# Performance work log

Hardware: AMD Instinct MI355X
Metric: run time of the kernel (lower is better)

Reference implementation:

```python
import jax, jax.numpy as jnp
import numpy as np

EPS = 1e-5

def conv2d(x, w, stride, pad):
    return jax.lax.conv_general_dilated(
        x, w, window_strides=(stride, stride),
        padding=[(pad, pad), (pad, pad)],
        dimension_numbers=('NCHW', 'OIHW', 'NCHW'))

def batchnorm(x, gamma, beta, mean, var):
    # inference-mode BN over channel dim of NCHW
    inv = jax.lax.rsqrt(var + EPS)
    return (x - mean[None, :, None, None]) * (inv * gamma)[None, :, None, None] + beta[None, :, None, None]

def rational(x, num, den):
    # Rational activation, version A, degrees (5,4):
    #   P(x) = num0 + num1*x + ... + num5*x^5  (Horner)
    #   Q(x) = 1 + sum_{j=1..4} |den_{j-1}| * |x|^j
    p = num[5]
    for i in range(4, -1, -1):
        p = p * x + num[i]
    xa = jnp.abs(x)
    q = jnp.ones_like(x)
    pw = xa
    for j in range(4):
        q = q + jnp.abs(den[j]) * pw
        pw = pw * xa
    return p / q

def multi_variant_rationals(out, num_r, den_r, num_g, den_g, num_b, den_b):
    # channels 0::3 -> r, 1::3 -> g, 2::3 -> b, then re-interleave
    B, C, H, W = out.shape
    o = out.reshape(B, C // 3, 3, H, W)  # channel c = 3*j + k
    r = rational(o[:, :, 0], num_r, den_r)
    g = rational(o[:, :, 1], num_g, den_g)
    b = rational(o[:, :, 2], num_b, den_b)
    return jnp.stack([r, g, b], axis=2).reshape(B, C, H, W)

def setup_inputs() -> dict:
    key = jax.random.key(0)
    ks = jax.random.split(key, 12)
    B, Cin, Cout, H, W = 64, 96, 192, 56, 56
    inp = {
        'x': jax.random.normal(ks[0], (B, Cin, H, W), jnp.float32),
        'w1': jax.random.normal(ks[1], (Cout, Cin, 3, 3), jnp.float32) * 0.05,
        'gamma1': jnp.ones((Cout,), jnp.float32),
        'beta1': jnp.zeros((Cout,), jnp.float32),
        'mean1': jnp.zeros((Cout,), jnp.float32),
        'var1': jnp.ones((Cout,), jnp.float32),
        'num_r': jax.random.normal(ks[2], (6,), jnp.float32) * 0.3,
        'den_r': jax.random.normal(ks[3], (4,), jnp.float32) * 0.3,
        'num_g': jax.random.normal(ks[4], (6,), jnp.float32) * 0.3,
        'den_g': jax.random.normal(ks[5], (4,), jnp.float32) * 0.3,
        'num_b': jax.random.normal(ks[6], (6,), jnp.float32) * 0.3,
        'den_b': jax.random.normal(ks[7], (4,), jnp.float32) * 0.3,
        'w2': jax.random.normal(ks[8], (Cout, Cout, 3, 3), jnp.float32) * 0.05,
        'gamma2': jnp.ones((Cout,), jnp.float32),
        'beta2': jnp.zeros((Cout,), jnp.float32),
        'mean2': jnp.zeros((Cout,), jnp.float32),
        'var2': jnp.ones((Cout,), jnp.float32),
        'ws': jax.random.normal(ks[9], (Cout, Cin, 1, 1), jnp.float32) * 0.05,
        'gammas': jnp.ones((Cout,), jnp.float32),
        'betas': jnp.zeros((Cout,), jnp.float32),
        'means': jnp.zeros((Cout,), jnp.float32),
        'vars_': jnp.ones((Cout,), jnp.float32),
    }
    return inp

def reference(x, w1, gamma1, beta1, mean1, var1,
              num_r, den_r, num_g, den_g, num_b, den_b,
              w2, gamma2, beta2, mean2, var2,
              ws, gammas, betas, means, vars_):
    STRIDE = 2
    out = batchnorm(conv2d(x, w1, STRIDE, 1), gamma1, beta1, mean1, var1)
    out = multi_variant_rationals(out, num_r, den_r, num_g, den_g, num_b, den_b)
    out = batchnorm(conv2d(out, w2, 1, 1), gamma2, beta2, mean2, var2)
    shortcut = batchnorm(conv2d(x, ws, STRIDE, 0), gammas, betas, means, vars_)
    out = out + shortcut
    out = multi_variant_rationals(out, num_r, den_r, num_g, den_g, num_b, den_b)
    return out
```

## Files before the change

kernel.cpp:

```cpp
#include <hip/hip_runtime.h>

#define EPSBN  1e-5f
#define NBLK_A 392
#define NBLK_B 392

#define W1B_OFF 0u
#define W2B_OFF 331776u
#define WSB_OFF 995328u
#define CS_OFF  1044480u
#define XT_OFF  1048320u
#define ACT_OFF 39583488u

typedef __attribute__((ext_vector_type(8))) short bf16x8;
typedef __attribute__((ext_vector_type(4))) short bf16x4;
typedef __attribute__((ext_vector_type(4))) float f32x4;

#define WAITV(N) asm volatile("s_waitcnt vmcnt(" #N ")" ::: "memory")

__device__ __forceinline__ short f2bf(float f) {
    unsigned u = __float_as_uint(f);
    u += 0x7fffu + ((u >> 16) & 1u);
    return (short)(u >> 16);
}

__device__ __forceinline__ void gload16(const short* g, short* l) {
    __builtin_amdgcn_global_load_lds(
        (const __attribute__((address_space(1))) void*)g,
        (__attribute__((address_space(3))) void*)l, 16, 0, 0);
}

__device__ __forceinline__ float rational_eval(float v, const float* nm, const float* dn) {
    float p = nm[5];
    p = p * v + nm[4];
    p = p * v + nm[3];
    p = p * v + nm[2];
    p = p * v + nm[1];
    p = p * v + nm[0];
    float xa = fabsf(v);
    float q = 1.0f;
    float pw = xa;
    q += dn[0] * pw; pw *= xa;
    q += dn[1] * pw; pw *= xa;
    q += dn[2] * pw; pw *= xa;
    q += dn[3] * pw;
    float inv = __builtin_amdgcn_rcpf(q);
    inv = inv * (2.0f - q * inv);
    return p * inv;
}

__device__ __forceinline__ void sel_coeffs(int v, const float cnm[3][6], const float cdn[3][4],
                                           float nm[6], float dn[4]) {
#pragma unroll
    for (int i = 0; i < 6; i++) nm[i] = (v == 0) ? cnm[0][i] : ((v == 1) ? cnm[1][i] : cnm[2][i]);
#pragma unroll
    for (int i = 0; i < 4; i++) dn[i] = (v == 0) ? cdn[0][i] : ((v == 1) ? cdn[1][i] : cdn[2][i]);
}

extern "C" __global__ __launch_bounds__(256)
void prep_all_kernel(
    const float* __restrict__ x,
    const float* __restrict__ w1, const float* __restrict__ w2, const float* __restrict__ wsc,
    const float* g1, const float* b1, const float* m1, const float* v1,
    const float* g2, const float* b2, const float* m2, const float* v2,
    const float* gs, const float* bs, const float* ms, const float* vs,
    short* __restrict__ w1t, short* __restrict__ w2t, short* __restrict__ wst,
    float* __restrict__ cs, short* __restrict__ act, short* __restrict__ xt)
{
    __shared__ float t[96 * 57];
    int blk = blockIdx.x;
    if (blk < 1296) {
        int i = blk * 256 + threadIdx.x;
        int u = i / 12288; int L = i - u * 12288;
        int row = L >> 6; int s = (L >> 3) & 7; int j = L & 7;
        int k = u * 64 + ((s ^ (row & 7)) << 3) + j;
        int kpos = k / 192; int ci = k - kpos * 192;
        float a = g2[row] * rsqrtf(v2[row] + EPSBN);
        w2t[i] = f2bf(w2[(row * 192 + ci) * 9 + kpos] * a);
    } else if (blk < 1944) {
        int i = (blk - 1296) * 256 + threadIdx.x;
        int u = i / 6144; int L = i - u * 6144;
        int row = L >> 5; int s = (L >> 3) & 3; int j = L & 7;
        int k = u * 32 + ((s ^ ((row >> 1) & 3)) << 3) + j;
        int kpos = k / 96; int ci = k - kpos * 96;
        float a = g1[row] * rsqrtf(v1[row] + EPSBN);
        w1t[i] = f2bf(w1[(row * 96 + ci) * 9 + kpos] * a);
    } else if (blk < 2040) {
        int i = (blk - 1944) * 256 + threadIdx.x;
        int u = i / 12288; int L = i - u * 12288;
        int row = L >> 6; int s = (L >> 3) & 7; int j = L & 7;
        int k = u * 64 + ((s ^ (row & 7)) << 3) + j;
        float a = gs[row] * rsqrtf(vs[row] + EPSBN);
        wst[i] = (k < 96) ? f2bf(wsc[row * 96 + k] * a) : (short)0;
    } else if (blk < 3432) {
        int i = (blk - 2040) * 256 + threadIdx.x;
        int c4 = i % 48;
        int tt = i / 48;
        int rp = tt % 116;
        int n = tt / 116;
        int h, w;
        if (rp < 30)      { h = 0;  w = rp; }
        else if (rp < 60) { h = 29; w = rp - 30; }
        else { int k = rp - 60; h = (k >> 1) + 1; w = (k & 1) ? 29 : 0; }
        *(bf16x4*)&act[((n * 30 + h) * 30 + w) * 192 + c4 * 4] = (bf16x4)(short)0;
    } else if (blk < 7016) {
        int b = blk - 3432;
        int n = b / 56, h = b - n * 56;
        const float* src = x + n * (96 * 3136) + h * 56;
        for (int i = threadIdx.x; i < 96 * 28; i += 256) {
            int c = i / 28, w2i = i - c * 28;
            float2 v = *(const float2*)&src[c * 3136 + w2i * 2];
            t[c * 57 + w2i * 2]     = v.x;
            t[c * 57 + w2i * 2 + 1] = v.y;
        }
        __syncthreads();
        unsigned* dst = (unsigned*)(xt + (n * 56 + h) * 56 * 96);
        for (int i = threadIdx.x; i < 56 * 24; i += 256) {
            int w = i / 24, cp2 = i - (i / 24) * 24;
            unsigned u0 = (unsigned short)f2bf(t[(4 * cp2 + 0) * 57 + w]);
            unsigned u1 = (unsigned short)f2bf(t[(4 * cp2 + 1) * 57 + w]);
            unsigned u2 = (unsigned short)f2bf(t[(4 * cp2 + 2) * 57 + w]);
            unsigned u3 = (unsigned short)f2bf(t[(4 * cp2 + 3) * 57 + w]);
            uint2 pk; pk.x = u0 | (u1 << 16); pk.y = u2 | (u3 << 16);
            *(uint2*)&dst[w * 48 + cp2 * 2] = pk;
        }
    } else {
        int i = threadIdx.x;
        if (i < 192) {
            float a1 = g1[i] * rsqrtf(v1[i] + EPSBN);
            float a2 = g2[i] * rsqrtf(v2[i] + EPSBN);
            float a3 = gs[i] * rsqrtf(vs[i] + EPSBN);
            cs[576 + i] = b1[i] - m1[i] * a1;
            cs[768 + i] = (b2[i] - m2[i] * a2) + (bs[i] - ms[i] * a3);
        }
    }
}

extern "C" __global__ __launch_bounds__(512, 4)
void convA_kernel(const short* __restrict__ xt,
                  const short* __restrict__ w1t,
                  const short* __restrict__ zbuf,
                  const float* __restrict__ bias1,
                  const float* __restrict__ num_r, const float* __restrict__ den_r,
                  const float* __restrict__ num_g, const float* __restrict__ den_g,
                  const float* __restrict__ num_b, const float* __restrict__ den_b,
                  short* __restrict__ act)
{
    __shared__ short lA[3][192 * 32];
    __shared__ short lB[3][128 * 32];

    const int tid  = threadIdx.x;
    const int lane = tid & 63;
    const int wave = tid >> 6;
    const int wm = wave >> 1, wn = wave & 1;
    const int lbid = (blockIdx.x & 7) * 49 + (blockIdx.x >> 3);
    const int p0   = lbid * 128;

    const int sA = (((tid & 3) ^ ((tid >> 3) & 3))) * 8;
    const int r1 = tid >> 2;

    int xb0; bool top, left;
    {
        int p = p0 + r1;
        int n = p / 784; int pr = p - n * 784;
        int oh = pr / 28; int ow = pr - oh * 28;
        xb0 = ((n * 56 + 2 * oh) * 56 + 2 * ow) * 96 + sA;
        top = (oh == 0); left = (ow == 0);
    }

    const int l15 = lane & 15, ksl = lane >> 4;
    int ard[3], brd[4];
#pragma unroll
    for (int m = 0; m < 3; ++m) {
        int row = wm * 48 + m * 16 + l15;
        ard[m] = row * 32 + ((ksl ^ ((row >> 1) & 3)) << 3);
    }
#pragma unroll
    for (int n = 0; n < 4; ++n) {
        int row = wn * 64 + n * 16 + l15;
        brd[n] = row * 32 + ((ksl ^ ((row >> 1) & 3)) << 3);
    }

    const int aoff = wave * 512 + lane * 8;

    auto stage = [&](int buf, int t) {
        const short* aw = &w1t[t * 6144 + aoff];
        gload16(aw, &lA[buf][wave * 512]);
        if (tid < 256) gload16(aw + 4096, &lA[buf][4096 + wave * 512]);
        int kpos = t / 3, cb = t - 3 * kpos;
        int kh = kpos / 3, kw = kpos - 3 * kh;
        int bko = ((kh - 1) * 56 + (kw - 1)) * 96 + cb * 32;
        const short* src = (((kh == 0) && top) || ((kw == 0) && left)) ? zbuf : &xt[xb0 + bko];
        gload16(src, &lB[buf][wave * 512]);
    };

    f32x4 acc[3][4];
#pragma unroll
    for (int m = 0; m < 3; m++)
#pragma unroll
        for (int n = 0; n < 4; n++) acc[m][n] = (f32x4){0.f, 0.f, 0.f, 0.f};

    stage(0, 0);
    stage(1, 1);
    WAITV(0);
    __builtin_amdgcn_s_barrier();

#pragma unroll
    for (int t = 0; t < 27; ++t) {
        const int cur = t % 3;
        if (t + 2 < 27) stage((t + 2) % 3, t + 2);
        bf16x8 af[3];
#pragma unroll
        for (int m = 0; m < 3; ++m) af[m] = *(const bf16x8*)&lA[cur][ard[m]];
        __builtin_amdgcn_s_setprio(1);
#pragma unroll
        for (int n = 0; n < 4; ++n) {
            bf16x8 bv = *(const bf16x8*)&lB[cur][brd[n]];
#pragma unroll
            for (int m = 0; m < 3; ++m)
                acc[m][n] = __builtin_amdgcn_mfma_f32_16x16x32_bf16(af[m], bv, acc[m][n], 0, 0, 0);
        }
        __builtin_amdgcn_s_setprio(0);
        if (t + 1 < 27) {
            if (t + 2 < 27) {
                if (wave < 4) { WAITV(3); } else { WAITV(2); }
            } else {
                WAITV(0);
            }
            __builtin_amdgcn_s_barrier();
        }
    }

    float cnm[3][6], cdn[3][4];
#pragma unroll
    for (int i = 0; i < 6; i++) { cnm[0][i] = num_r[i]; cnm[1][i] = num_g[i]; cnm[2][i] = num_b[i]; }
#pragma unroll
    for (int i = 0; i < 4; i++) { cdn[0][i] = fabsf(den_r[i]); cdn[1][i] = fabsf(den_g[i]); cdn[2][i] = fabsf(den_b[i]); }

    int abase[4];
#pragma unroll
    for (int n = 0; n < 4; ++n) {
        int pp = p0 + wn * 64 + n * 16 + l15;
        int n2 = pp / 784; int r2 = pp - n2 * 784;
        int oh2 = r2 / 28; int ow2 = r2 - oh2 * 28;
        abase[n] = ((n2 * 30 + oh2 + 1) * 30 + ow2 + 1) * 192;
    }
#pragma unroll
    for (int m = 0; m < 3; ++m) {
        int cob = wm * 48 + m * 16 + (ksl << 2);
        float res[4][4];
#pragma unroll
        for (int r = 0; r < 4; ++r) {
            float nm[6], dn[4];
            sel_coeffs((cob + r) % 3, cnm, cdn, nm, dn);
            float bv = bias1[cob + r];
#pragma unroll
            for (int n = 0; n < 4; ++n)
                res[n][r] = rational_eval(acc[m][n][r] + bv, nm, dn);
        }
#pragma unroll
        for (int n = 0; n < 4; ++n) {
            bf16x4 pk;
#pragma unroll
            for (int r = 0; r < 4; ++r) pk[r] = f2bf(res[n][r]);
            *(bf16x4*)&act[abase[n] + cob] = pk;
        }
    }
}

extern "C" __global__ __launch_bounds__(512, 4)
void convB_kernel(const short* __restrict__ act,
                  const short* __restrict__ xt,
                  const short* __restrict__ w2t,
                  const short* __restrict__ wst,
                  const float* __restrict__ bias2s,
                  const float* __restrict__ num_r, const float* __restrict__ den_r,
                  const float* __restrict__ num_g, const float* __restrict__ den_g,
                  const float* __restrict__ num_b, const float* __restrict__ den_b,
                  float* __restrict__ outp)
{
    __shared__ short lA[2][192 * 64];
    __shared__ short lB[2][128 * 64];

    const int tid  = threadIdx.x;
    const int lane = tid & 63;
    const int wave = tid >> 6;
    const int wm = wave >> 1, wn = wave & 1;
    const int lbid = (blockIdx.x & 7) * 49 + (blockIdx.x >> 3);
    const int p0   = lbid * 128;

    const int s8 = (((tid & 7) ^ ((tid >> 3) & 7))) * 8;
    const int rA = tid >> 3;

    int abB[2], xcB[2];
#pragma unroll
    for (int c = 0; c < 2; ++c) {
        int p = p0 + c * 64 + rA;
        int n = p / 784; int pr = p - n * 784;
        int oh = pr / 28; int ow = pr - oh * 28;
        abB[c] = ((n * 30 + oh) * 30 + ow) * 192 + s8;
        xcB[c] = ((n * 56 + 2 * oh) * 56 + 2 * ow) * 96 + s8;
    }

    const int l15 = lane & 15, ksl = lane >> 4;
    int ard[2][3], brd[2][4];
#pragma unroll
    for (int kk = 0; kk < 2; ++kk) {
#pragma unroll
        for (int m = 0; m < 3; ++m) {
            int row = wm * 48 + m * 16 + l15;
            ard[kk][m] = row * 64 + ((((kk << 2) | ksl) ^ (row & 7)) << 3);
        }
#pragma unroll
        for (int n = 0; n < 4; ++n) {
            int row = wn * 64 + n * 16 + l15;
            brd[kk][n] = row * 64 + ((((kk << 2) | ksl) ^ (row & 7)) << 3);
        }
    }

    const int aoff = wave * 512 + lane * 8;

    auto stage = [&](int buf, int t) {
        if (t < 2) {
            const short* aw = &wst[t * 12288 + aoff];
#pragma unroll
            for (int c = 0; c < 3; ++c)
                gload16(aw + c * 4096, &lA[buf][c * 4096 + wave * 512]);
#pragma unroll
            for (int c = 0; c < 2; ++c)
                gload16(&xt[xcB[c] + t * 64], &lB[buf][c * 4096 + wave * 512]);
        } else {
            int u = t - 2;
            const short* aw = &w2t[u * 12288 + aoff];
#pragma unroll
            for (int c = 0; c < 3; ++c)
                gload16(aw + c * 4096, &lA[buf][c * 4096 + wave * 512]);
            int kpos = u / 3, cb = u - 3 * kpos;
            int kh = kpos / 3, kw = kpos - 3 * kh;
            int bko = (kh * 30 + kw) * 192 + cb * 64;
#pragma unroll
            for (int c = 0; c < 2; ++c)
                gload16(&act[abB[c] + bko], &lB[buf][c * 4096 + wave * 512]);
        }
    };

    f32x4 acc[3][4];
#pragma unroll
    for (int m = 0; m < 3; m++)
#pragma unroll
        for (int n = 0; n < 4; n++) acc[m][n] = (f32x4){0.f, 0.f, 0.f, 0.f};

    stage(0, 0);
    int cur = 0;
    for (int t = 0; t < 29; ++t) {
        __syncthreads();
        if (t + 1 < 29) stage(cur ^ 1, t + 1);
        __builtin_amdgcn_s_setprio(1);
#pragma unroll
        for (int kk = 0; kk < 2; ++kk) {
            bf16x8 af[3];
#pragma unroll
            for (int m = 0; m < 3; ++m) af[m] = *(const bf16x8*)&lA[cur][ard[kk][m]];
#pragma unroll
            for (int n = 0; n < 4; ++n) {
                bf16x8 bv = *(const bf16x8*)&lB[cur][brd[kk][n]];
#pragma unroll
                for (int m = 0; m < 3; ++m)
                    acc[m][n] = __builtin_amdgcn_mfma_f32_16x16x32_bf16(af[m], bv, acc[m][n], 0, 0, 0);
            }
        }
        __builtin_amdgcn_s_setprio(0);
        cur ^= 1;
    }

    float cnm[3][6], cdn[3][4];
#pragma unroll
    for (int i = 0; i < 6; i++) { cnm[0][i] = num_r[i]; cnm[1][i] = num_g[i]; cnm[2][i] = num_b[i]; }
#pragma unroll
    for (int i = 0; i < 4; i++) { cdn[0][i] = fabsf(den_r[i]); cdn[1][i] = fabsf(den_g[i]); cdn[2][i] = fabsf(den_b[i]); }

    int obase[4];
#pragma unroll
    for (int n = 0; n < 4; ++n) {
        int pp = p0 + wn * 64 + n * 16 + l15;
        int n2 = pp / 784; int r2 = pp - n2 * 784;
        int oh2 = r2 / 28; int ow2 = r2 - oh2 * 28;
        obase[n] = n2 * (192 * 784) + oh2 * 28 + ow2;
    }
#pragma unroll
    for (int m = 0; m < 3; ++m) {
        int cob = wm * 48 + m * 16 + (ksl << 2);
#pragma unroll
        for (int r = 0; r < 4; ++r) {
            float nm[6], dn[4];
            sel_coeffs((cob + r) % 3, cnm, cdn, nm, dn);
            float bv = bias2s[cob + r];
#pragma unroll
            for (int n = 0; n < 4; ++n) {
                int idx = obase[n] + (cob + r) * 784;
                outp[idx] = rational_eval(acc[m][n][r] + bv, nm, dn);
            }
        }
    }
}

extern "C" void kernel_launch(void* const* d_in, const int* in_sizes, int n_in,
                              void* d_out, int out_size, void* d_ws, size_t ws_size,
                              hipStream_t stream)
{
    const float* x      = (const float*)d_in[0];
    const float* w1     = (const float*)d_in[1];
    const float* gamma1 = (const float*)d_in[2];
    const float* beta1  = (const float*)d_in[3];
    const float* mean1  = (const float*)d_in[4];
    const float* var1   = (const float*)d_in[5];
    const float* num_r  = (const float*)d_in[6];
    const float* den_r  = (const float*)d_in[7];
    const float* num_g  = (const float*)d_in[8];
    const float* den_g  = (const float*)d_in[9];
    const float* num_b  = (const float*)d_in[10];
    const float* den_b  = (const float*)d_in[11];
    const float* w2     = (const float*)d_in[12];
    const float* gamma2 = (const float*)d_in[13];
    const float* beta2  = (const float*)d_in[14];
    const float* mean2  = (const float*)d_in[15];
    const float* var2   = (const float*)d_in[16];
    const float* wsc    = (const float*)d_in[17];
    const float* gammas = (const float*)d_in[18];
    const float* betas  = (const float*)d_in[19];
    const float* means  = (const float*)d_in[20];
    const float* vars_  = (const float*)d_in[21];

    char* base = (char*)d_ws;
    short* w1t  = (short*)(base + W1B_OFF);
    short* w2t  = (short*)(base + W2B_OFF);
    short* wst  = (short*)(base + WSB_OFF);
    float* cs   = (float*)(base + CS_OFF);
    short* xt   = (short*)(base + XT_OFF);
    short* act  = (short*)(base + ACT_OFF);
    float* outp = (float*)d_out;

    float* bias1  = cs + 576;
    float* bias2s = cs + 768;
    const short* zbuf = wst + 12288 + 32;

    prep_all_kernel<<<7017, 256, 0, stream>>>(x, w1, w2, wsc,
                                              gamma1, beta1, mean1, var1,
                                              gamma2, beta2, mean2, var2,
                                              gammas, betas, means, vars_,
                                              w1t, w2t, wst, cs, act, xt);

    convA_kernel<<<NBLK_A, 512, 0, stream>>>(xt, w1t, zbuf, bias1,
                                             num_r, den_r, num_g, den_g, num_b, den_b,
                                             act);

    convB_kernel<<<NBLK_B, 512, 0, stream>>>(act, xt, w2t, wst, bias2s,
                                             num_r, den_r, num_g, den_g, num_b, den_b,
                                             outp);
}
```

Before: 123.9 us.

## Widen convA K-step to 64, drop padded act buffer via zero-region offsets

convA now stages K in chunks of 64 (14 steps, double-buffered with syncthreads) instead of 32 (27 steps, triple-buffered with hand-tuned vmcnt waits). Per-tap gather offsets are precomputed, and out-of-bounds taps point into a zeroed region of the workspace. The intermediate activation tensor changes from a zero-padded 30x30 layout to an unpadded 28x28 one, so prep no longer needs blocks to zero the border. convB gathers through per-tap offsets with the same zero-address trick. The aim is fewer barriers and loop iterations and less prep work, at the cost of larger LDS footprint and more registers for offset tables.

```diff
diff --git a/kernel.cpp b/kernel.cpp
--- a/kernel.cpp
+++ b/kernel.cpp
@@ -4,18 +4,19 @@
 #define NBLK_A 392
 #define NBLK_B 392
 
-#define W1B_OFF 0u
-#define W2B_OFF 331776u
-#define WSB_OFF 995328u
-#define CS_OFF  1044480u
-#define XT_OFF  1048320u
-#define ACT_OFF 39583488u
+#define W1T_OFF 0u
+#define W2T_OFF 344064u
+#define WST_OFF 1007616u
+#define CS_OFF  1056768u
+#define XT_OFF  1058816u
+#define ACT_OFF 39593984u
+
+#define ZXT   (-256)
+#define ZACT  (-19267840)
 
 typedef __attribute__((ext_vector_type(8))) short bf16x8;
 typedef __attribute__((ext_vector_type(4))) short bf16x4;
 typedef __attribute__((ext_vector_type(4))) float f32x4;
-
-#define WAITV(N) asm volatile("s_waitcnt vmcnt(" #N ")" ::: "memory")
 
 __device__ __forceinline__ short f2bf(float f) {
     unsigned u = __float_as_uint(f);
@@ -64,7 +65,7 @@
     const float* g2, const float* b2, const float* m2, const float* v2,
     const float* gs, const float* bs, const float* ms, const float* vs,
     short* __restrict__ w1t, short* __restrict__ w2t, short* __restrict__ wst,
-    float* __restrict__ cs, short* __restrict__ act, short* __restrict__ xt)
+    float* __restrict__ cs, short* __restrict__ xt)
 {
     __shared__ float t[96 * 57];
     int blk = blockIdx.x;
@@ -76,34 +77,27 @@
         int kpos = k / 192; int ci = k - kpos * 192;
         float a = g2[row] * rsqrtf(v2[row] + EPSBN);
         w2t[i] = f2bf(w2[(row * 192 + ci) * 9 + kpos] * a);
-    } else if (blk < 1944) {
+    } else if (blk < 1968) {
         int i = (blk - 1296) * 256 + threadIdx.x;
-        int u = i / 6144; int L = i - u * 6144;
-        int row = L >> 5; int s = (L >> 3) & 3; int j = L & 7;
-        int k = u * 32 + ((s ^ ((row >> 1) & 3)) << 3) + j;
-        int kpos = k / 96; int ci = k - kpos * 96;
-        float a = g1[row] * rsqrtf(v1[row] + EPSBN);
-        w1t[i] = f2bf(w1[(row * 96 + ci) * 9 + kpos] * a);
-    } else if (blk < 2040) {
-        int i = (blk - 1944) * 256 + threadIdx.x;
+        int u = i / 12288; int L = i - u * 12288;
+        int row = L >> 6; int s = (L >> 3) & 7; int j = L & 7;
+        int k = u * 64 + ((s ^ (row & 7)) << 3) + j;
+        short val = 0;
+        if (k < 864) {
+            int kpos = k / 96; int ci = k - kpos * 96;
+            float a = g1[row] * rsqrtf(v1[row] + EPSBN);
+            val = f2bf(w1[(row * 96 + ci) * 9 + kpos] * a);
+        }
+        w1t[i] = val;
+    } else if (blk < 2064) {
+        int i = (blk - 1968) * 256 + threadIdx.x;
         int u = i / 12288; int L = i - u * 12288;
         int row = L >> 6; int s = (L >> 3) & 7; int j = L & 7;
         int k = u * 64 + ((s ^ (row & 7)) << 3) + j;
         float a = gs[row] * rsqrtf(vs[row] + EPSBN);
         wst[i] = (k < 96) ? f2bf(wsc[row * 96 + k] * a) : (short)0;
-    } else if (blk < 3432) {
-        int i = (blk - 2040) * 256 + threadIdx.x;
-        int c4 = i % 48;
-        int tt = i / 48;
-        int rp = tt % 116;
-        int n = tt / 116;
-        int h, w;
-        if (rp < 30)      { h = 0;  w = rp; }
-        else if (rp < 60) { h = 29; w = rp - 30; }
-        else { int k = rp - 60; h = (k >> 1) + 1; w = (k & 1) ? 29 : 0; }
-        *(bf16x4*)&act[((n * 30 + h) * 30 + w) * 192 + c4 * 4] = (bf16x4)(short)0;
-    } else if (blk < 7016) {
-        int b = blk - 3432;
+    } else if (blk < 5648) {
+        int b = blk - 2064;
         int n = b / 56, h = b - n * 56;
         const float* src = x + n * (96 * 3136) + h * 56;
         for (int i = threadIdx.x; i < 96 * 28; i += 256) {
@@ -129,8 +123,10 @@
             float a1 = g1[i] * rsqrtf(v1[i] + EPSBN);
             float a2 = g2[i] * rsqrtf(v2[i] + EPSBN);
             float a3 = gs[i] * rsqrtf(vs[i] + EPSBN);
-            cs[576 + i] = b1[i] - m1[i] * a1;
-            cs[768 + i] = (b2[i] - m2[i] * a2) + (bs[i] - ms[i] * a3);
+            cs[i]       = b1[i] - m1[i] * a1;
+            cs[192 + i] = (b2[i] - m2[i] * a2) + (bs[i] - ms[i] * a3);
+        } else if (i < 320) {
+            cs[384 + (i - 192)] = 0.f;
         }
     }
 }
@@ -138,15 +134,14 @@
 extern "C" __global__ __launch_bounds__(512, 4)
 void convA_kernel(const short* __restrict__ xt,
                   const short* __restrict__ w1t,
-                  const short* __restrict__ zbuf,
                   const float* __restrict__ bias1,
                   const float* __restrict__ num_r, const float* __restrict__ den_r,
                   const float* __restrict__ num_g, const float* __restrict__ den_g,
                   const float* __restrict__ num_b, const float* __restrict__ den_b,
                   short* __restrict__ act)
 {
-    __shared__ short lA[3][192 * 32];
-    __shared__ short lB[3][128 * 32];
+    __shared__ short lA[2][192 * 64];
+    __shared__ short lB[2][128 * 64];
 
     const int tid  = threadIdx.x;
     const int lane = tid & 63;
@@ -155,80 +150,90 @@
     const int lbid = (blockIdx.x & 7) * 49 + (blockIdx.x >> 3);
     const int p0   = lbid * 128;
 
-    const int sA = (((tid & 3) ^ ((tid >> 3) & 3))) * 8;
-    const int r1 = tid >> 2;
-
-    int xb0; bool top, left;
-    {
-        int p = p0 + r1;
+    const int s8 = (((tid & 7) ^ ((tid >> 3) & 7))) * 8;
+    const int rA = tid >> 3;
+    const bool c32 = (s8 < 32);
+
+    int adjvs[2][10];
+#pragma unroll
+    for (int c = 0; c < 2; ++c) {
+        int p = p0 + c * 64 + rA;
         int n = p / 784; int pr = p - n * 784;
         int oh = pr / 28; int ow = pr - oh * 28;
-        xb0 = ((n * 56 + 2 * oh) * 56 + 2 * ow) * 96 + sA;
-        top = (oh == 0); left = (ow == 0);
+#pragma unroll
+        for (int tap = 0; tap < 9; ++tap) {
+            int kh = tap / 3, kw = tap - 3 * kh;
+            int ih = 2 * oh + kh - 1, iw = 2 * ow + kw - 1;
+            bool valid = (ih >= 0) && (iw >= 0);
+            int base = ((n * 56 + ih) * 56 + iw) * 96;
+            adjvs[c][tap] = (valid ? base : ZXT) - 96 * tap + s8;
+        }
+        adjvs[c][9] = ZXT - 864 + s8;
     }
 
     const int l15 = lane & 15, ksl = lane >> 4;
-    int ard[3], brd[4];
-#pragma unroll
-    for (int m = 0; m < 3; ++m) {
-        int row = wm * 48 + m * 16 + l15;
-        ard[m] = row * 32 + ((ksl ^ ((row >> 1) & 3)) << 3);
-    }
-#pragma unroll
-    for (int n = 0; n < 4; ++n) {
-        int row = wn * 64 + n * 16 + l15;
-        brd[n] = row * 32 + ((ksl ^ ((row >> 1) & 3)) << 3);
+    int ard[2][3], brd[2][4];
+#pragma unroll
+    for (int kk = 0; kk < 2; ++kk) {
+#pragma unroll
+        for (int m = 0; m < 3; ++m) {
+            int row = wm * 48 + m * 16 + l15;
+            ard[kk][m] = row * 64 + ((((kk << 2) | ksl) ^ (row & 7)) << 3);
+        }
+#pragma unroll
+        for (int n = 0; n < 4; ++n) {
+            int row = wn * 64 + n * 16 + l15;
+            brd[kk][n] = row * 64 + ((((kk << 2) | ksl) ^ (row & 7)) << 3);
+        }
     }
 
     const int aoff = wave * 512 + lane * 8;
 
-    auto stage = [&](int buf, int t) {
-        const short* aw = &w1t[t * 6144 + aoff];
-        gload16(aw, &lA[buf][wave * 512]);
-        if (tid < 256) gload16(aw + 4096, &lA[buf][4096 + wave * 512]);
-        int kpos = t / 3, cb = t - 3 * kpos;
-        int kh = kpos / 3, kw = kpos - 3 * kh;
-        int bko = ((kh - 1) * 56 + (kw - 1)) * 96 + cb * 32;
-        const short* src = (((kh == 0) && top) || ((kw == 0) && left)) ? zbuf : &xt[xb0 + bko];
-        gload16(src, &lB[buf][wave * 512]);
-    };
-
     f32x4 acc[3][4];
 #pragma unroll
     for (int m = 0; m < 3; m++)
 #pragma unroll
         for (int n = 0; n < 4; n++) acc[m][n] = (f32x4){0.f, 0.f, 0.f, 0.f};
 
-    stage(0, 0);
-    stage(1, 1);
-    WAITV(0);
-    __builtin_amdgcn_s_barrier();
-
-#pragma unroll
-    for (int t = 0; t < 27; ++t) {
-        const int cur = t % 3;
-        if (t + 2 < 27) stage((t + 2) % 3, t + 2);
-        bf16x8 af[3];
-#pragma unroll
-        for (int m = 0; m < 3; ++m) af[m] = *(const bf16x8*)&lA[cur][ard[m]];
+    const int LO[14] = {0,0,1,2,2,3,4,4,5,6,6,7,8,8};
+    const int HI[14] = {0,1,1,2,3,3,4,5,5,6,7,7,8,9};
+
+#define STAGE_A(buf, t_)                                                                    \
+    do {                                                                                    \
+        const int t__ = (t_);                                                               \
+        const short* aw = &w1t[t__ * 12288 + aoff];                                         \
+        _Pragma("unroll") for (int c3 = 0; c3 < 3; ++c3)                                    \
+            gload16(aw + c3 * 4096, &lA[buf][c3 * 4096 + wave * 512]);                      \
+        _Pragma("unroll") for (int c = 0; c < 2; ++c) {                                     \
+            int av = (LO[t__] == HI[t__]) ? adjvs[c][LO[t__]]                               \
+                     : (c32 ? adjvs[c][LO[t__]] : adjvs[c][HI[t__]]);                       \
+            gload16(&xt[av + t__ * 64], &lB[buf][c * 4096 + wave * 512]);                   \
+        }                                                                                   \
+    } while (0)
+
+    STAGE_A(0, 0);
+#pragma unroll
+    for (int t = 0; t < 14; ++t) {
+        const int cur = t & 1;
+        __syncthreads();
+        if (t + 1 < 14) STAGE_A(cur ^ 1, t + 1);
         __builtin_amdgcn_s_setprio(1);
 #pragma unroll
-        for (int n = 0; n < 4; ++n) {
-            bf16x8 bv = *(const bf16x8*)&lB[cur][brd[n]];
-#pragma unroll
-            for (int m = 0; m < 3; ++m)
-                acc[m][n] = __builtin_amdgcn_mfma_f32_16x16x32_bf16(af[m], bv, acc[m][n], 0, 0, 0);
+        for (int kk = 0; kk < 2; ++kk) {
+            bf16x8 af[3];
+#pragma unroll
+            for (int m = 0; m < 3; ++m) af[m] = *(const bf16x8*)&lA[cur][ard[kk][m]];
+#pragma unroll
+            for (int n = 0; n < 4; ++n) {
+                bf16x8 bv = *(const bf16x8*)&lB[cur][brd[kk][n]];
+#pragma unroll
+                for (int m = 0; m < 3; ++m)
+                    acc[m][n] = __builtin_amdgcn_mfma_f32_16x16x32_bf16(af[m], bv, acc[m][n], 0, 0, 0);
+            }
         }
         __builtin_amdgcn_s_setprio(0);
-        if (t + 1 < 27) {
-            if (t + 2 < 27) {
-                if (wave < 4) { WAITV(3); } else { WAITV(2); }
-            } else {
-                WAITV(0);
-            }
-            __builtin_amdgcn_s_barrier();
-        }
-    }
+    }
+#undef STAGE_A
 
     float cnm[3][6], cdn[3][4];
 #pragma unroll
@@ -242,7 +247,7 @@
         int pp = p0 + wn * 64 + n * 16 + l15;
         int n2 = pp / 784; int r2 = pp - n2 * 784;
         int oh2 = r2 / 28; int ow2 = r2 - oh2 * 28;
-        abase[n] = ((n2 * 30 + oh2 + 1) * 30 + ow2 + 1) * 192;
+        abase[n] = ((n2 * 28 + oh2) * 28 + ow2) * 192;
     }
 #pragma unroll
     for (int m = 0; m < 3; ++m) {
@@ -291,14 +296,21 @@
     const int s8 = (((tid & 7) ^ ((tid >> 3) & 7))) * 8;
     const int rA = tid >> 3;
 
-    int abB[2], xcB[2];
+    int adjB[2][9], xcB[2];
 #pragma unroll
     for (int c = 0; c < 2; ++c) {
         int p = p0 + c * 64 + rA;
         int n = p / 784; int pr = p - n * 784;
         int oh = pr / 28; int ow = pr - oh * 28;
-        abB[c] = ((n * 30 + oh) * 30 + ow) * 192 + s8;
         xcB[c] = ((n * 56 + 2 * oh) * 56 + 2 * ow) * 96 + s8;
+#pragma unroll
+        for (int tap = 0; tap < 9; ++tap) {
+            int kh = tap / 3, kw = tap - 3 * kh;
+            int ih = oh + kh - 1, iw = ow + kw - 1;
+            bool valid = (ih >= 0) && (ih < 28) && (iw >= 0) && (iw < 28);
+            int base = ((n * 28 + ih) * 28 + iw) * 192;
+            adjB[c][tap] = (valid ? base : ZACT) + s8;
+        }
     }
 
     const int l15 = lane & 15, ksl = lane >> 4;
@@ -319,29 +331,25 @@
 
     const int aoff = wave * 512 + lane * 8;
 
-    auto stage = [&](int buf, int t) {
-        if (t < 2) {
-            const short* aw = &wst[t * 12288 + aoff];
-#pragma unroll
-            for (int c = 0; c < 3; ++c)
-                gload16(aw + c * 4096, &lA[buf][c * 4096 + wave * 512]);
-#pragma unroll
-            for (int c = 0; c < 2; ++c)
-                gload16(&xt[xcB[c] + t * 64], &lB[buf][c * 4096 + wave * 512]);
-        } else {
-            int u = t - 2;
-            const short* aw = &w2t[u * 12288 + aoff];
-#pragma unroll
-            for (int c = 0; c < 3; ++c)
-                gload16(aw + c * 4096, &lA[buf][c * 4096 + wave * 512]);
-            int kpos = u / 3, cb = u - 3 * kpos;
-            int kh = kpos / 3, kw = kpos - 3 * kh;
-            int bko = (kh * 30 + kw) * 192 + cb * 64;
-#pragma unroll
-            for (int c = 0; c < 2; ++c)
-                gload16(&act[abB[c] + bko], &lB[buf][c * 4096 + wave * 512]);
-        }
-    };
+#define STAGE_B(buf, t_)                                                                    \
+    do {                                                                                    \
+        const int t__ = (t_);                                                               \
+        if (t__ < 2) {                                                                      \
+            const short* aw = &wst[t__ * 12288 + aoff];                                     \
+            _Pragma("unroll") for (int c3 = 0; c3 < 3; ++c3)                                \
+                gload16(aw + c3 * 4096, &lA[buf][c3 * 4096 + wave * 512]);                  \
+            _Pragma("unroll") for (int c = 0; c < 2; ++c)                                   \
+                gload16(&xt[xcB[c] + t__ * 64], &lB[buf][c * 4096 + wave * 512]);           \
+        } else {                                                                            \
+            const int u__ = t__ - 2;                                                        \
+            const int tap__ = u__ / 3, cb__ = u__ - 3 * tap__;                              \
+            const short* aw = &w2t[u__ * 12288 + aoff];                                     \
+            _Pragma("unroll") for (int c3 = 0; c3 < 3; ++c3)                                \
+                gload16(aw + c3 * 4096, &lA[buf][c3 * 4096 + wave * 512]);                  \
+            _Pragma("unroll") for (int c = 0; c < 2; ++c)                                   \
+                gload16(&act[adjB[c][tap__] + cb__ * 64], &lB[buf][c * 4096 + wave * 512]); \
+        }                                                                                   \
+    } while (0)
 
     f32x4 acc[3][4];
 #pragma unroll
@@ -349,11 +357,12 @@
 #pragma unroll
         for (int n = 0; n < 4; n++) acc[m][n] = (f32x4){0.f, 0.f, 0.f, 0.f};
 
-    stage(0, 0);
-    int cur = 0;
+    STAGE_B(0, 0);
+#pragma unroll
     for (int t = 0; t < 29; ++t) {
+        const int cur = t & 1;
         __syncthreads();
-        if (t + 1 < 29) stage(cur ^ 1, t + 1);
+        if (t + 1 < 29) STAGE_B(cur ^ 1, t + 1);
         __builtin_amdgcn_s_setprio(1);
 #pragma unroll
         for (int kk = 0; kk < 2; ++kk) {
@@ -369,8 +378,8 @@
             }
         }
         __builtin_amdgcn_s_setprio(0);
-        cur ^= 1;
-    }
+    }
+#undef STAGE_B
 
     float cnm[3][6], cdn[3][4];
 #pragma unroll
@@ -431,25 +440,24 @@
     const float* vars_  = (const float*)d_in[21];
 
     char* base = (char*)d_ws;
-    short* w1t  = (short*)(base + W1B_OFF);
-    short* w2t  = (short*)(base + W2B_OFF);
-    short* wst  = (short*)(base + WSB_OFF);
+    short* w1t  = (short*)(base + W1T_OFF);
+    short* w2t  = (short*)(base + W2T_OFF);
+    short* wst  = (short*)(base + WST_OFF);
     float* cs   = (float*)(base + CS_OFF);
     short* xt   = (short*)(base + XT_OFF);
     short* act  = (short*)(base + ACT_OFF);
     float* outp = (float*)d_out;
 
-    float* bias1  = cs + 576;
-    float* bias2s = cs + 768;
-    const short* zbuf = wst + 12288 + 32;
-
-    prep_all_kernel<<<7017, 256, 0, stream>>>(x, w1, w2, wsc,
+    float* bias1  = cs;
+    float* bias2s = cs + 192;
+
+    prep_all_kernel<<<5649, 256, 0, stream>>>(x, w1, w2, wsc,
                                               gamma1, beta1, mean1, var1,
                                               gamma2, beta2, mean2, var2,
                                               gammas, betas, means, vars_,
-                                              w1t, w2t, wst, cs, act, xt);
-
-    convA_kernel<<<NBLK_A, 512, 0, stream>>>(xt, w1t, zbuf, bias1,
+                                              w1t, w2t, wst, cs, xt);
+
+    convA_kernel<<<NBLK_A, 512, 0, stream>>>(xt, w1t, bias1,
                                              num_r, den_r, num_g, den_g, num_b, den_b,
                                              act);
 
```

Result: no change. 124.8 us (+0.8%).
